# Optimization experiments

Measured on AMD Instinct MI355X. Metric: run time of the kernel, lower is better.

Reference implementation:

```python
import jax, jax.numpy as jnp
import numpy as np

N_QUBITS = 8

def _ry(theta):
    # PennyLane RY = exp(-i theta Y/2) = [[c,-s],[s,c]]
    c = jnp.cos(theta / 2).astype(jnp.complex64)
    s = jnp.sin(theta / 2).astype(jnp.complex64)
    return jnp.stack([jnp.stack([c, -s], -1), jnp.stack([s, c], -1)], -2)

def _rz(theta):
    # PennyLane RZ = diag(e^{-i theta/2}, e^{i theta/2})
    ph = jnp.exp(-0.5j * theta.astype(jnp.complex64))
    z = jnp.zeros_like(ph)
    return jnp.stack([jnp.stack([ph, z], -1), jnp.stack([z, jnp.conj(ph)], -1)], -2)

def _apply_1q(state, U, wire):
    # state: (B, 2,...,2); U: (2,2) or (B,2,2)
    state = jnp.moveaxis(state, wire + 1, -1)
    if U.ndim == 3:
        state = jnp.einsum('bij,b...j->b...i', U, state)
    else:
        state = jnp.einsum('ij,b...j->b...i', U, state)
    return jnp.moveaxis(state, -1, wire + 1)

def _apply_cnot(state, c, t):
    state = jnp.moveaxis(state, (c + 1, t + 1), (-2, -1))
    state = jnp.concatenate([state[..., 0:1, :], state[..., 1:2, ::-1]], axis=-2)
    return jnp.moveaxis(state, (-2, -1), (c + 1, t + 1))

def _circuit(angles, qw):
    # angles: (B, 2*n_qubits), qw: (3, n_qubits, 3)
    B = angles.shape[0]
    state = jnp.zeros((B,) + (2,) * N_QUBITS, jnp.complex64)
    state = state.at[(slice(None),) + (0,) * N_QUBITS].set(1.0)
    for i in range(N_QUBITS):
        state = _apply_1q(state, _ry(angles[:, i]), i)
        state = _apply_1q(state, _rz(angles[:, i + N_QUBITS]), i)
    for layer in range(3):
        for i in range(N_QUBITS):
            phi, theta, omega = qw[layer, i]
            U = _rz(omega) @ _ry(theta) @ _rz(phi)  # Rot(phi,theta,omega)
            state = _apply_1q(state, U, i)
        for i in range(N_QUBITS - 1):
            state = _apply_cnot(state, i, i + 1)
        state = _apply_cnot(state, N_QUBITS - 1, 0)
    probs = jnp.abs(state) ** 2  # (B, 2,...,2) real
    expz = []
    for i in range(N_QUBITS):
        p = probs.sum(axis=tuple(a for a in range(1, N_QUBITS + 1) if a != i + 1))
        expz.append(p[:, 0] - p[:, 1])  # <Z_i> = p(0) - p(1)
    return jnp.stack(expz, -1)


def setup_inputs() -> dict:
    key = jax.random.key(0)
    ks = jax.random.split(key, 10)
    B = 16384
    return {
        'x': jax.random.normal(ks[0], (B, 80), jnp.float32),
        'W1': jax.random.normal(ks[1], (64, 80), jnp.float32) * 0.1,
        'b1': jax.random.normal(ks[2], (64,), jnp.float32) * 0.1,
        'W2': jax.random.normal(ks[3], (32, 64), jnp.float32) * 0.1,
        'b2': jax.random.normal(ks[4], (32,), jnp.float32) * 0.1,
        'W3': jax.random.normal(ks[5], (16, 32), jnp.float32) * 0.1,
        'b3': jax.random.normal(ks[6], (16,), jnp.float32) * 0.1,
        'qw': jax.random.normal(ks[7], (3, 8, 3), jnp.float32),
        'Wp': jax.random.normal(ks[8], (128, 8), jnp.float32) * 0.1,
        'bp': jax.random.normal(ks[9], (128,), jnp.float32) * 0.1,
    }


def reference(x, W1, b1, W2, b2, W3, b3, qw, Wp, bp):
    h = jnp.tanh(x @ W1.T + b1)
    h = jnp.tanh(h @ W2.T + b2)
    angles = h @ W3.T + b3          # (B, 16)
    z = _circuit(angles, qw)        # (B, 8) PauliZ expectations
    return z @ Wp.T + bp            # (B, 128)
```

## Files before the change

### kernel.cpp

```cpp
#include <hip/hip_runtime.h>

typedef float v2f __attribute__((ext_vector_type(2)));

#define WPB 4

__device__ __forceinline__ float xorf(float v, int sb) {
  return __int_as_float(__float_as_int(v) ^ sb);
}

__device__ __forceinline__ void pkfma_ip(v2f a, v2f b, v2f& acc) {
  asm("v_pk_fma_f32 %0, %1, %2, %0" : "+v"(acc) : "v"(a), "v"(b));
}
__device__ __forceinline__ v2f pkmul_bl(v2f c, v2f v) {
  v2f r; asm("v_pk_mul_f32 %0, %1, %2 op_sel:[0,0] op_sel_hi:[0,1]"
             : "=v"(r) : "v"(c), "v"(v)); return r;
}
__device__ __forceinline__ void pkfma_bl(v2f c, v2f v, v2f& acc) {
  asm("v_pk_fma_f32 %0, %1, %2, %0 op_sel:[0,0,0] op_sel_hi:[0,1,1]"
      : "+v"(acc) : "v"(c), "v"(v));
}
__device__ __forceinline__ void pkfma_bl_n(v2f c, v2f v, v2f& acc) {
  asm("v_pk_fma_f32 %0, %1, %2, %0 op_sel:[0,0,0] op_sel_hi:[0,1,1] neg_lo:[1,0,0] neg_hi:[1,0,0]"
      : "+v"(acc) : "v"(c), "v"(v));
}
__device__ __forceinline__ void pkfma_bh_i(v2f c, v2f v, v2f& acc) {
  asm("v_pk_fma_f32 %0, %1, %2, %0 op_sel:[1,1,0] op_sel_hi:[1,0,1] neg_lo:[1,0,0]"
      : "+v"(acc) : "v"(c), "v"(v));
}
__device__ __forceinline__ void pkfma_bh_mi(v2f c, v2f v, v2f& acc) {
  asm("v_pk_fma_f32 %0, %1, %2, %0 op_sel:[1,1,0] op_sel_hi:[1,0,1] neg_hi:[1,0,0]"
      : "+v"(acc) : "v"(c), "v"(v));
}
__device__ __forceinline__ v2f cmul(v2f a, v2f b) {
  v2f r = pkmul_bl(a, b);
  pkfma_bh_i(a, b, r);
  return r;
}

template<int M>
__device__ __forceinline__ float xch(float v, int a32) {
  if constexpr (M == 32)
    return __int_as_float(__builtin_amdgcn_ds_bpermute(a32, __float_as_int(v)));
  else if constexpr (M == 16 || M == 4)
    return __int_as_float(__builtin_amdgcn_ds_swizzle(__float_as_int(v), (M << 10) | 0x1f));
  else if constexpr (M == 8) {
    int i = __float_as_int(v);
    return __int_as_float(__builtin_amdgcn_update_dpp(i, i, 0x128, 0xF, 0xF, false));
  } else if constexpr (M == 2) {
    int i = __float_as_int(v);
    return __int_as_float(__builtin_amdgcn_update_dpp(i, i, 0x4E, 0xF, 0xF, false));
  } else {
    int i = __float_as_int(v);
    return __int_as_float(__builtin_amdgcn_update_dpp(i, i, 0xB1, 0xF, 0xF, false));
  }
}
template<int M>
__device__ __forceinline__ v2f xch2(v2f v, int a32) {
  v2f r; r.x = xch<M>(v.x, a32); r.y = xch<M>(v.y, a32); return r;
}
__device__ __forceinline__ v2f bperm2(int addr, v2f v) {
  v2f r;
  r.x = __int_as_float(__builtin_amdgcn_ds_bpermute(addr, __float_as_int(v.x)));
  r.y = __int_as_float(__builtin_amdgcn_ds_bpermute(addr, __float_as_int(v.y)));
  return r;
}

__device__ __forceinline__ void gpair(v2f& a, v2f& b, v2f P1, v2f P2) {
  v2f na = pkmul_bl(P1, a);
  pkfma_bh_i(P1, a, na);
  pkfma_bl(P2, b, na);
  pkfma_bh_i(P2, b, na);
  v2f nb = pkmul_bl(P1, b);
  pkfma_bh_mi(P1, b, nb);
  pkfma_bl_n(P2, a, nb);
  pkfma_bh_i(P2, a, nb);
  a = na; b = nb;
}
__device__ __forceinline__ v2f glane(v2f a, v2f p, v2f P1, v2f P2) {
  v2f t = pkmul_bl(P1, a);
  pkfma_bh_i(P1, a, t);
  pkfma_bl(P2, p, t);
  pkfma_bh_i(P2, p, t);
  return t;
}

template<int W>
__device__ __forceinline__ void gate_both(v2f* SA, v2f* SB, v2f P1, v2f P2,
                                          const int* sb, int a32) {
  if constexpr (W == 0) {
    gpair(SA[0], SA[2], P1, P2); gpair(SA[1], SA[3], P1, P2);
    gpair(SB[0], SB[2], P1, P2); gpair(SB[1], SB[3], P1, P2);
  } else if constexpr (W == 1) {
    gpair(SA[0], SA[1], P1, P2); gpair(SA[2], SA[3], P1, P2);
    gpair(SB[0], SB[1], P1, P2); gpair(SB[2], SB[3], P1, P2);
  } else {
    constexpr int M = 1 << (7 - W);
    const int s = sb[W - 2];
    v2f P1s = P1; P1s.y = xorf(P1.y, s);
    v2f P2s = P2; P2s.x = xorf(P2.x, s);
    v2f pa0 = xch2<M>(SA[0], a32), pa1 = xch2<M>(SA[1], a32),
        pa2 = xch2<M>(SA[2], a32), pa3 = xch2<M>(SA[3], a32);
    v2f pb0 = xch2<M>(SB[0], a32), pb1 = xch2<M>(SB[1], a32),
        pb2 = xch2<M>(SB[2], a32), pb3 = xch2<M>(SB[3], a32);
    SA[0] = glane(SA[0], pa0, P1s, P2s); SA[1] = glane(SA[1], pa1, P1s, P2s);
    SA[2] = glane(SA[2], pa2, P1s, P2s); SA[3] = glane(SA[3], pa3, P1s, P2s);
    SB[0] = glane(SB[0], pb0, P1s, P2s); SB[1] = glane(SB[1], pb1, P1s, P2s);
    SB[2] = glane(SB[2], pb2, P1s, P2s); SB[3] = glane(SB[3], pb3, P1s, P2s);
  }
}

__device__ __forceinline__ void build_state(v2f* S, const float4* csW, int lane) {
  v2f g[6];
  #pragma unroll
  for (int w = 2; w < 8; ++w) {
    float4 c = csW[w];
    v2f P1 = (v2f){c.x, c.y};
    v2f nc2 = (v2f){-c.z, c.w};
    bool shi = ((lane >> (7 - w)) & 1) != 0;
    g[w - 2] = shi ? nc2 : P1;
  }
  v2f c23 = cmul(g[0], g[1]);
  v2f c45 = cmul(g[2], g[3]);
  v2f c67 = cmul(g[4], g[5]);
  v2f common = cmul(c23, cmul(c45, c67));
  float4 c0 = csW[0], c1 = csW[1];
  v2f P10 = (v2f){c0.x, c0.y}, m0 = (v2f){-c0.z, c0.w};
  v2f P11 = (v2f){c1.x, c1.y}, m1 = (v2f){-c1.z, c1.w};
  S[0] = cmul(cmul(P10, P11), common);
  S[1] = cmul(cmul(P10, m1 ), common);
  S[2] = cmul(cmul(m0 , P11), common);
  S[3] = cmul(cmul(m0 , m1 ), common);
}

__device__ __forceinline__ void cnot_ring(v2f* S, int addrA, int addrB, int lane) {
  { v2f t = S[2]; S[2] = S[3]; S[3] = t; }
  S[0] = bperm2(addrA, S[0]); S[2] = bperm2(addrA, S[2]);
  S[1] = bperm2(addrB, S[1]); S[3] = bperm2(addrB, S[3]);
  bool c0 = (lane & 1) != 0;
  v2f t0 = S[0], t1 = S[1];
  S[0] = c0 ? S[2] : S[0]; S[2] = c0 ? t0 : S[2];
  S[1] = c0 ? S[3] : S[1]; S[3] = c0 ? t1 : S[3];
}

__device__ __forceinline__ void readout(const v2f* S, int lane, const int* sb,
                                        int a32, float* z) {
  float p0 = S[0].x*S[0].x + S[0].y*S[0].y;
  float p1 = S[1].x*S[1].x + S[1].y*S[1].y;
  float p2 = S[2].x*S[2].x + S[2].y*S[2].y;
  float p3 = S[3].x*S[3].x + S[3].y*S[3].y;
  float E = (p0 + p3) - (p1 + p2);
  float F = (p0 + p2) - (p1 + p3);
  float Fv = xorf(F, (__popc(lane) & 1) << 31);
  float Sm = E, d1, d2, d3, d4, d5, d6;
  { float p = xch<32>(Sm, a32); d1 = xorf(Sm - p, sb[0]); Sm += p; }
  { float p = xch<16>(Sm, a32); Sm += p;
    float q = xch<16>(d1, a32); d2 = xorf(d1 - q, sb[1]); d1 += q; }
  { float p = xch<8>(Sm, a32); Sm += p;
    float q = xch<8>(d1, a32); d1 += q;
    float r = xch<8>(d2, a32); d3 = xorf(d2 - r, sb[2]); d2 += r; }
  { float p = xch<4>(Sm, a32); Sm += p;
    float q = xch<4>(d1, a32); d1 += q;
    float r = xch<4>(d2, a32); d2 += r;
    float t = xch<4>(d3, a32); d4 = xorf(d3 - t, sb[3]); d3 += t; }
  { float p = xch<2>(Sm, a32); Sm += p;
    float q = xch<2>(d1, a32); d1 += q;
    float r = xch<2>(d2, a32); d2 += r;
    float t = xch<2>(d3, a32); d3 += t;
    float w = xch<2>(d4, a32); d5 = xorf(d4 - w, sb[4]); d4 += w; }
  { float p = xch<1>(Sm, a32); Sm += p;
    float q = xch<1>(d1, a32); d1 += q;
    float r = xch<1>(d2, a32); d2 += r;
    float t = xch<1>(d3, a32); d3 += t;
    float w = xch<1>(d4, a32); d4 += w;
    float v = xch<1>(d5, a32); d6 = xorf(d5 - v, sb[5]); d5 += v; }
  Fv += xch<32>(Fv, a32); Fv += xch<16>(Fv, a32); Fv += xch<8>(Fv, a32);
  Fv += xch<4>(Fv, a32);  Fv += xch<2>(Fv, a32);  Fv += xch<1>(Fv, a32);
  z[0] = Fv; z[1] = Sm; z[2] = d1; z[3] = d2;
  z[4] = d3; z[5] = d4; z[6] = d5; z[7] = d6;
}

__device__ __forceinline__ float fast_tanh(float x) {
  float e = __expf(2.f * x);
  return 1.f - 2.f * __builtin_amdgcn_rcpf(e + 1.f);
}
__device__ __forceinline__ v2f vlo(float4 v) { return (v2f){v.x, v.y}; }
__device__ __forceinline__ v2f vhi(float4 v) { return (v2f){v.z, v.w}; }

__global__ void prep_rot_kernel(const float* __restrict__ qw, float* __restrict__ U) {
  int t = threadIdx.x;
  if (t < 24) {
    float phi = qw[t*3+0], theta = qw[t*3+1], omega = qw[t*3+2];
    float st, ct; sincosf(0.5f*theta, &st, &ct);
    float sa, ca; sincosf(0.5f*(phi+omega), &sa, &ca);
    float sd, cd; sincosf(0.5f*(phi-omega), &sd, &cd);
    float4 o; o.x = ct*ca; o.y = -ct*sa; o.z = -st*cd; o.w = -st*sd;
    ((float4*)U)[t] = o;
  }
}

__global__ __launch_bounds__(64*WPB) void qblock_kernel(
    const float* __restrict__ x,  const float* __restrict__ W1, const float* __restrict__ b1,
    const float* __restrict__ W2, const float* __restrict__ b2,
    const float* __restrict__ W3, const float* __restrict__ b3,
    const float* __restrict__ Urot, const float* __restrict__ Wp, const float* __restrict__ bp,
    float* __restrict__ out, int B2)
{
  __shared__ float  h1s[WPB][2][64];
  __shared__ float  h2s[WPB][2][32];
  __shared__ v2f    cs [WPB][2][16];
  __shared__ float4 csW[WPB][2][8];

  const int lane = threadIdx.x & 63;
  const int wv   = threadIdx.x >> 6;
  int bw = blockIdx.x * WPB + wv;
  if (bw >= B2) bw = B2 - 1;
  bw = __builtin_amdgcn_readfirstlane(bw);
  const int e0 = 2 * bw, e1 = e0 + 1;
  const v2f* Ug2 = (const v2f*)Urot;

  {
    const float4* xv0 = (const float4*)(x + (size_t)e0 * 80);
    const float4* xv1 = (const float4*)(x + (size_t)e1 * 80);
    const float4* wr  = (const float4*)(W1 + lane * 80);
    float bv = b1[lane];
    v2f a00 = (v2f){bv, 0.f}, a01 = (v2f){0.f, 0.f};
    v2f a10 = (v2f){bv, 0.f}, a11 = (v2f){0.f, 0.f};
    #pragma unroll
    for (int k = 0; k < 20; ++k) {
      float4 wk = wr[k], x0 = xv0[k], x1 = xv1[k];
      pkfma_ip(vlo(x0), vlo(wk), a00); pkfma_ip(vhi(x0), vhi(wk), a01);
      pkfma_ip(vlo(x1), vlo(wk), a10); pkfma_ip(vhi(x1), vhi(wk), a11);
    }
    h1s[wv][0][lane] = fast_tanh((a00.x + a00.y) + (a01.x + a01.y));
    h1s[wv][1][lane] = fast_tanh((a10.x + a10.y) + (a11.x + a11.y));
  }
  __threadfence_block();

  {
    const int e = lane >> 5, row = lane & 31;
    const float4* hv = (const float4*)(&h1s[wv][e][0]);
    const float4* wr = (const float4*)(W2 + row * 64);
    v2f ac0 = (v2f){b2[row], 0.f}, ac1 = (v2f){0.f, 0.f};
    #pragma unroll
    for (int k = 0; k < 16; ++k) {
      float4 hk = hv[k], wk = wr[k];
      pkfma_ip(vlo(hk), vlo(wk), ac0);
      pkfma_ip(vhi(hk), vhi(wk), ac1);
    }
    h2s[wv][e][row] = fast_tanh((ac0.x + ac0.y) + (ac1.x + ac1.y));
  }
  __threadfence_block();

  if (lane < 32) {
    const int e = lane >> 4, row = lane & 15;
    const float4* hv = (const float4*)(&h2s[wv][e][0]);
    const float4* wr = (const float4*)(W3 + row * 32);
    v2f ac0 = (v2f){b3[row], 0.f}, ac1 = (v2f){0.f, 0.f};
    #pragma unroll
    for (int k = 0; k < 8; ++k) {
      float4 hk = hv[k], wk = wr[k];
      pkfma_ip(vlo(hk), vlo(wk), ac0);
      pkfma_ip(vhi(hk), vhi(wk), ac1);
    }
    float sh, ch; __sincosf(0.5f * ((ac0.x + ac0.y) + (ac1.x + ac1.y)), &sh, &ch);
    cs[wv][e][row] = (v2f){ch, sh};
  }
  __threadfence_block();

  if (lane < 32) {
    const int e = lane >> 4, k = lane & 15;
    if (k < 8) {
      v2f yy = cs[wv][e][k], zz = cs[wv][e][k + 8];
      v2f u1 = (v2f){  yy.x * zz.x, -yy.x * zz.y };
      v2f u2 = (v2f){ -yy.y * zz.x,  yy.y * zz.y };
      v2f cu1 = (v2f){ u1.x, -u1.y };
      v2f cu2 = (v2f){ u2.x, -u2.y };
      v2f r1 = Ug2[2 * k], r2 = Ug2[2 * k + 1];
      v2f P1c = cmul(r1, u1);
      pkfma_bl_n(r2, cu2, P1c);
      pkfma_bh_mi(r2, cu2, P1c);
      v2f P2c = cmul(r1, u2);
      pkfma_bl(r2, cu1, P2c);
      pkfma_bh_i(r2, cu1, P2c);
      csW[wv][e][k] = make_float4(P1c.x, P1c.y, P2c.x, P2c.y);
    }
  }
  __threadfence_block();

  const int a32 = (lane ^ 32) << 2;
  const int sb[6] = { (lane&32)<<26, (lane&16)<<27, (lane&8)<<28,
                      (lane&4)<<29, (lane&2)<<30, (lane&1)<<31 };
  const int addrA = ((lane ^ (lane >> 1)) & 63) << 2;
  const int addrB = addrA ^ 128;

  v2f SA[4], SB[4];
  build_state(SA, &csW[wv][0][0], lane);
  build_state(SB, &csW[wv][1][0], lane);
  cnot_ring(SA, addrA, addrB, lane); cnot_ring(SB, addrA, addrB, lane);

  #define LGB(l, i) { v2f P1 = Ug2[((l)*8+(i))*2], P2 = Ug2[((l)*8+(i))*2+1]; \
    gate_both<i>(SA, SB, P1, P2, sb, a32); }
  LGB(1,0) LGB(1,1) LGB(1,2) LGB(1,3) LGB(1,4) LGB(1,5) LGB(1,6) LGB(1,7)
  cnot_ring(SA, addrA, addrB, lane); cnot_ring(SB, addrA, addrB, lane);
  LGB(2,0) LGB(2,1) LGB(2,2) LGB(2,3) LGB(2,4) LGB(2,5) LGB(2,6) LGB(2,7)
  #undef LGB

  float zA[8], zB[8];
  readout(SA, lane, sb, a32, zA);
  readout(SB, lane, sb, a32, zB);

  const int r0 = 2 * lane;
  const float4* wp = (const float4*)(Wp + r0 * 8);
  float4 w0v = wp[0], w1v = wp[1], w2v = wp[2], w3v = wp[3];
  float2 bpv = ((const float2*)bp)[lane];
  {
    float o0 = bpv.x + zA[0]*w0v.x + zA[1]*w0v.y + zA[2]*w0v.z + zA[3]*w0v.w
                     + zA[4]*w1v.x + zA[5]*w1v.y + zA[6]*w1v.z + zA[7]*w1v.w;
    float o1 = bpv.y + zA[0]*w2v.x + zA[1]*w2v.y + zA[2]*w2v.z + zA[3]*w2v.w
                     + zA[4]*w3v.x + zA[5]*w3v.y + zA[6]*w3v.z + zA[7]*w3v.w;
    ((float2*)(out + (size_t)e0 * 128))[lane] = make_float2(o0, o1);
  }
  {
    float o0 = bpv.x + zB[0]*w0v.x + zB[1]*w0v.y + zB[2]*w0v.z + zB[3]*w0v.w
                     + zB[4]*w1v.x + zB[5]*w1v.y + zB[6]*w1v.z + zB[7]*w1v.w;
    float o1 = bpv.y + zB[0]*w2v.x + zB[1]*w2v.y + zB[2]*w2v.z + zB[3]*w2v.w
                     + zB[4]*w3v.x + zB[5]*w3v.y + zB[6]*w3v.z + zB[7]*w3v.w;
    ((float2*)(out + (size_t)e1 * 128))[lane] = make_float2(o0, o1);
  }
}

extern "C" void kernel_launch(void* const* d_in, const int* in_sizes, int n_in,
                              void* d_out, int out_size, void* d_ws, size_t ws_size,
                              hipStream_t stream) {
  const float* x  = (const float*)d_in[0];
  const float* W1 = (const float*)d_in[1];
  const float* b1 = (const float*)d_in[2];
  const float* W2 = (const float*)d_in[3];
  const float* b2 = (const float*)d_in[4];
  const float* W3 = (const float*)d_in[5];
  const float* b3 = (const float*)d_in[6];
  const float* qw = (const float*)d_in[7];
  const float* Wp = (const float*)d_in[8];
  const float* bp = (const float*)d_in[9];
  float* out = (float*)d_out;
  float* Urot = (float*)d_ws;

  const int B = in_sizes[0] / 80;
  const int B2 = B / 2;
  prep_rot_kernel<<<1, 64, 0, stream>>>(qw, Urot);
  const int grid = (B2 + WPB - 1) / WPB;
  qblock_kernel<<<grid, 64 * WPB, 0, stream>>>(x, W1, b1, W2, b2, W3, b3,
                                               Urot, Wp, bp, out, B2);
}
```

Baseline: 47.88 us.

## Process four batch elements per wavefront instead of two

Each wavefront now simulates four circuits at once, widening per-lane state to 16 complex pairs. The first MLP layer reuses each W1 row load across four samples, and later stages use all lanes instead of half. This is meant to amortize weight loads and gate-parameter broadcasts and to add independent work for latency hiding. It raises register pressure, may reduce occupancy, and halves the grid size.

```diff
diff --git a/kernel.cpp b/kernel.cpp
--- a/kernel.cpp
+++ b/kernel.cpp
@@ -3,6 +3,7 @@
 typedef float v2f __attribute__((ext_vector_type(2)));
 
 #define WPB 4
+#define NE  4
 
 __device__ __forceinline__ float xorf(float v, int sb) {
   return __int_as_float(__float_as_int(v) ^ sb);
@@ -85,27 +86,32 @@
 }
 
 template<int W>
-__device__ __forceinline__ void gate_both(v2f* SA, v2f* SB, v2f P1, v2f P2,
-                                          const int* sb, int a32) {
+__device__ __forceinline__ void gate_all(v2f* S, v2f P1, v2f P2,
+                                         const int* sb, int a32) {
   if constexpr (W == 0) {
-    gpair(SA[0], SA[2], P1, P2); gpair(SA[1], SA[3], P1, P2);
-    gpair(SB[0], SB[2], P1, P2); gpair(SB[1], SB[3], P1, P2);
+    #pragma unroll
+    for (int e = 0; e < NE; ++e) {
+      gpair(S[4*e+0], S[4*e+2], P1, P2); gpair(S[4*e+1], S[4*e+3], P1, P2);
+    }
   } else if constexpr (W == 1) {
-    gpair(SA[0], SA[1], P1, P2); gpair(SA[2], SA[3], P1, P2);
-    gpair(SB[0], SB[1], P1, P2); gpair(SB[2], SB[3], P1, P2);
+    #pragma unroll
+    for (int e = 0; e < NE; ++e) {
+      gpair(S[4*e+0], S[4*e+1], P1, P2); gpair(S[4*e+2], S[4*e+3], P1, P2);
+    }
   } else {
     constexpr int M = 1 << (7 - W);
     const int s = sb[W - 2];
     v2f P1s = P1; P1s.y = xorf(P1.y, s);
     v2f P2s = P2; P2s.x = xorf(P2.x, s);
-    v2f pa0 = xch2<M>(SA[0], a32), pa1 = xch2<M>(SA[1], a32),
-        pa2 = xch2<M>(SA[2], a32), pa3 = xch2<M>(SA[3], a32);
-    v2f pb0 = xch2<M>(SB[0], a32), pb1 = xch2<M>(SB[1], a32),
-        pb2 = xch2<M>(SB[2], a32), pb3 = xch2<M>(SB[3], a32);
-    SA[0] = glane(SA[0], pa0, P1s, P2s); SA[1] = glane(SA[1], pa1, P1s, P2s);
-    SA[2] = glane(SA[2], pa2, P1s, P2s); SA[3] = glane(SA[3], pa3, P1s, P2s);
-    SB[0] = glane(SB[0], pb0, P1s, P2s); SB[1] = glane(SB[1], pb1, P1s, P2s);
-    SB[2] = glane(SB[2], pb2, P1s, P2s); SB[3] = glane(SB[3], pb3, P1s, P2s);
+    #pragma unroll
+    for (int e = 0; e < NE; ++e) {
+      v2f p0 = xch2<M>(S[4*e+0], a32), p1 = xch2<M>(S[4*e+1], a32),
+          p2 = xch2<M>(S[4*e+2], a32), p3 = xch2<M>(S[4*e+3], a32);
+      S[4*e+0] = glane(S[4*e+0], p0, P1s, P2s);
+      S[4*e+1] = glane(S[4*e+1], p1, P1s, P2s);
+      S[4*e+2] = glane(S[4*e+2], p2, P1s, P2s);
+      S[4*e+3] = glane(S[4*e+3], p3, P1s, P2s);
+    }
   }
 }
 
@@ -203,55 +209,62 @@
     const float* __restrict__ W2, const float* __restrict__ b2,
     const float* __restrict__ W3, const float* __restrict__ b3,
     const float* __restrict__ Urot, const float* __restrict__ Wp, const float* __restrict__ bp,
-    float* __restrict__ out, int B2)
+    float* __restrict__ out, int B4)
 {
-  __shared__ float  h1s[WPB][2][64];
-  __shared__ float  h2s[WPB][2][32];
-  __shared__ v2f    cs [WPB][2][16];
-  __shared__ float4 csW[WPB][2][8];
+  __shared__ float  h1s[WPB][NE][64];
+  __shared__ float  h2s[WPB][NE][32];
+  __shared__ v2f    cs [WPB][NE][16];
+  __shared__ float4 csW[WPB][NE][8];
 
   const int lane = threadIdx.x & 63;
   const int wv   = threadIdx.x >> 6;
   int bw = blockIdx.x * WPB + wv;
-  if (bw >= B2) bw = B2 - 1;
+  if (bw >= B4) bw = B4 - 1;
   bw = __builtin_amdgcn_readfirstlane(bw);
-  const int e0 = 2 * bw, e1 = e0 + 1;
+  const int e0 = NE * bw;
   const v2f* Ug2 = (const v2f*)Urot;
 
   {
-    const float4* xv0 = (const float4*)(x + (size_t)e0 * 80);
-    const float4* xv1 = (const float4*)(x + (size_t)e1 * 80);
-    const float4* wr  = (const float4*)(W1 + lane * 80);
+    const float4* wr = (const float4*)(W1 + lane * 80);
     float bv = b1[lane];
-    v2f a00 = (v2f){bv, 0.f}, a01 = (v2f){0.f, 0.f};
-    v2f a10 = (v2f){bv, 0.f}, a11 = (v2f){0.f, 0.f};
+    v2f a0[NE], a1[NE];
+    #pragma unroll
+    for (int e = 0; e < NE; ++e) { a0[e] = (v2f){bv, 0.f}; a1[e] = (v2f){0.f, 0.f}; }
     #pragma unroll
     for (int k = 0; k < 20; ++k) {
-      float4 wk = wr[k], x0 = xv0[k], x1 = xv1[k];
-      pkfma_ip(vlo(x0), vlo(wk), a00); pkfma_ip(vhi(x0), vhi(wk), a01);
-      pkfma_ip(vlo(x1), vlo(wk), a10); pkfma_ip(vhi(x1), vhi(wk), a11);
-    }
-    h1s[wv][0][lane] = fast_tanh((a00.x + a00.y) + (a01.x + a01.y));
-    h1s[wv][1][lane] = fast_tanh((a10.x + a10.y) + (a11.x + a11.y));
+      float4 wk = wr[k];
+      #pragma unroll
+      for (int e = 0; e < NE; ++e) {
+        float4 xk = ((const float4*)(x + (size_t)(e0 + e) * 80))[k];
+        pkfma_ip(vlo(xk), vlo(wk), a0[e]);
+        pkfma_ip(vhi(xk), vhi(wk), a1[e]);
+      }
+    }
+    #pragma unroll
+    for (int e = 0; e < NE; ++e)
+      h1s[wv][e][lane] = fast_tanh((a0[e].x + a0[e].y) + (a1[e].x + a1[e].y));
   }
   __threadfence_block();
 
   {
-    const int e = lane >> 5, row = lane & 31;
-    const float4* hv = (const float4*)(&h1s[wv][e][0]);
+    const int ep = lane >> 5, row = lane & 31;
     const float4* wr = (const float4*)(W2 + row * 64);
-    v2f ac0 = (v2f){b2[row], 0.f}, ac1 = (v2f){0.f, 0.f};
+    const float4* hvA = (const float4*)(&h1s[wv][2*ep+0][0]);
+    const float4* hvB = (const float4*)(&h1s[wv][2*ep+1][0]);
+    v2f aA0 = (v2f){b2[row], 0.f}, aA1 = (v2f){0.f, 0.f};
+    v2f aB0 = aA0, aB1 = aA1;
     #pragma unroll
     for (int k = 0; k < 16; ++k) {
-      float4 hk = hv[k], wk = wr[k];
-      pkfma_ip(vlo(hk), vlo(wk), ac0);
-      pkfma_ip(vhi(hk), vhi(wk), ac1);
-    }
-    h2s[wv][e][row] = fast_tanh((ac0.x + ac0.y) + (ac1.x + ac1.y));
+      float4 wk = wr[k], hA = hvA[k], hB = hvB[k];
+      pkfma_ip(vlo(hA), vlo(wk), aA0); pkfma_ip(vhi(hA), vhi(wk), aA1);
+      pkfma_ip(vlo(hB), vlo(wk), aB0); pkfma_ip(vhi(hB), vhi(wk), aB1);
+    }
+    h2s[wv][2*ep+0][row] = fast_tanh((aA0.x + aA0.y) + (aA1.x + aA1.y));
+    h2s[wv][2*ep+1][row] = fast_tanh((aB0.x + aB0.y) + (aB1.x + aB1.y));
   }
   __threadfence_block();
 
-  if (lane < 32) {
+  {
     const int e = lane >> 4, row = lane & 15;
     const float4* hv = (const float4*)(&h2s[wv][e][0]);
     const float4* wr = (const float4*)(W3 + row * 32);
@@ -268,22 +281,20 @@
   __threadfence_block();
 
   if (lane < 32) {
-    const int e = lane >> 4, k = lane & 15;
-    if (k < 8) {
-      v2f yy = cs[wv][e][k], zz = cs[wv][e][k + 8];
-      v2f u1 = (v2f){  yy.x * zz.x, -yy.x * zz.y };
-      v2f u2 = (v2f){ -yy.y * zz.x,  yy.y * zz.y };
-      v2f cu1 = (v2f){ u1.x, -u1.y };
-      v2f cu2 = (v2f){ u2.x, -u2.y };
-      v2f r1 = Ug2[2 * k], r2 = Ug2[2 * k + 1];
-      v2f P1c = cmul(r1, u1);
-      pkfma_bl_n(r2, cu2, P1c);
-      pkfma_bh_mi(r2, cu2, P1c);
-      v2f P2c = cmul(r1, u2);
-      pkfma_bl(r2, cu1, P2c);
-      pkfma_bh_i(r2, cu1, P2c);
-      csW[wv][e][k] = make_float4(P1c.x, P1c.y, P2c.x, P2c.y);
-    }
+    const int e = lane >> 3, k = lane & 7;
+    v2f yy = cs[wv][e][k], zz = cs[wv][e][k + 8];
+    v2f u1 = (v2f){  yy.x * zz.x, -yy.x * zz.y };
+    v2f u2 = (v2f){ -yy.y * zz.x,  yy.y * zz.y };
+    v2f cu1 = (v2f){ u1.x, -u1.y };
+    v2f cu2 = (v2f){ u2.x, -u2.y };
+    v2f r1 = Ug2[2 * k], r2 = Ug2[2 * k + 1];
+    v2f P1c = cmul(r1, u1);
+    pkfma_bl_n(r2, cu2, P1c);
+    pkfma_bh_mi(r2, cu2, P1c);
+    v2f P2c = cmul(r1, u2);
+    pkfma_bl(r2, cu1, P2c);
+    pkfma_bh_i(r2, cu1, P2c);
+    csW[wv][e][k] = make_float4(P1c.x, P1c.y, P2c.x, P2c.y);
   }
   __threadfence_block();
 
@@ -293,39 +304,33 @@
   const int addrA = ((lane ^ (lane >> 1)) & 63) << 2;
   const int addrB = addrA ^ 128;
 
-  v2f SA[4], SB[4];
-  build_state(SA, &csW[wv][0][0], lane);
-  build_state(SB, &csW[wv][1][0], lane);
-  cnot_ring(SA, addrA, addrB, lane); cnot_ring(SB, addrA, addrB, lane);
+  v2f S[4 * NE];
+  #pragma unroll
+  for (int e = 0; e < NE; ++e) build_state(&S[4*e], &csW[wv][e][0], lane);
+  #pragma unroll
+  for (int e = 0; e < NE; ++e) cnot_ring(&S[4*e], addrA, addrB, lane);
 
   #define LGB(l, i) { v2f P1 = Ug2[((l)*8+(i))*2], P2 = Ug2[((l)*8+(i))*2+1]; \
-    gate_both<i>(SA, SB, P1, P2, sb, a32); }
+    gate_all<i>(S, P1, P2, sb, a32); }
   LGB(1,0) LGB(1,1) LGB(1,2) LGB(1,3) LGB(1,4) LGB(1,5) LGB(1,6) LGB(1,7)
-  cnot_ring(SA, addrA, addrB, lane); cnot_ring(SB, addrA, addrB, lane);
+  #pragma unroll
+  for (int e = 0; e < NE; ++e) cnot_ring(&S[4*e], addrA, addrB, lane);
   LGB(2,0) LGB(2,1) LGB(2,2) LGB(2,3) LGB(2,4) LGB(2,5) LGB(2,6) LGB(2,7)
   #undef LGB
-
-  float zA[8], zB[8];
-  readout(SA, lane, sb, a32, zA);
-  readout(SB, lane, sb, a32, zB);
 
   const int r0 = 2 * lane;
   const float4* wp = (const float4*)(Wp + r0 * 8);
   float4 w0v = wp[0], w1v = wp[1], w2v = wp[2], w3v = wp[3];
   float2 bpv = ((const float2*)bp)[lane];
-  {
-    float o0 = bpv.x + zA[0]*w0v.x + zA[1]*w0v.y + zA[2]*w0v.z + zA[3]*w0v.w
-                     + zA[4]*w1v.x + zA[5]*w1v.y + zA[6]*w1v.z + zA[7]*w1v.w;
-    float o1 = bpv.y + zA[0]*w2v.x + zA[1]*w2v.y + zA[2]*w2v.z + zA[3]*w2v.w
-                     + zA[4]*w3v.x + zA[5]*w3v.y + zA[6]*w3v.z + zA[7]*w3v.w;
-    ((float2*)(out + (size_t)e0 * 128))[lane] = make_float2(o0, o1);
-  }
-  {
-    float o0 = bpv.x + zB[0]*w0v.x + zB[1]*w0v.y + zB[2]*w0v.z + zB[3]*w0v.w
-                     + zB[4]*w1v.x + zB[5]*w1v.y + zB[6]*w1v.z + zB[7]*w1v.w;
-    float o1 = bpv.y + zB[0]*w2v.x + zB[1]*w2v.y + zB[2]*w2v.z + zB[3]*w2v.w
-                     + zB[4]*w3v.x + zB[5]*w3v.y + zB[6]*w3v.z + zB[7]*w3v.w;
-    ((float2*)(out + (size_t)e1 * 128))[lane] = make_float2(o0, o1);
+  #pragma unroll
+  for (int e = 0; e < NE; ++e) {
+    float z[8];
+    readout(&S[4*e], lane, sb, a32, z);
+    float o0 = bpv.x + z[0]*w0v.x + z[1]*w0v.y + z[2]*w0v.z + z[3]*w0v.w
+                     + z[4]*w1v.x + z[5]*w1v.y + z[6]*w1v.z + z[7]*w1v.w;
+    float o1 = bpv.y + z[0]*w2v.x + z[1]*w2v.y + z[2]*w2v.z + z[3]*w2v.w
+                     + z[4]*w3v.x + z[5]*w3v.y + z[6]*w3v.z + z[7]*w3v.w;
+    ((float2*)(out + (size_t)(e0 + e) * 128))[lane] = make_float2(o0, o1);
   }
 }
 
@@ -346,9 +351,9 @@
   float* Urot = (float*)d_ws;
 
   const int B = in_sizes[0] / 80;
-  const int B2 = B / 2;
+  const int B4 = B / NE;
   prep_rot_kernel<<<1, 64, 0, stream>>>(qw, Urot);
-  const int grid = (B2 + WPB - 1) / WPB;
+  const int grid = (B4 + WPB - 1) / WPB;
   qblock_kernel<<<grid, 64 * WPB, 0, stream>>>(x, W1, b1, W2, b2, W3, b3,
-                                               Urot, Wp, bp, out, B2);
-}
+                                               Urot, Wp, bp, out, B4);
+}
```

New measurement: 42.20 us. 11.9% less time.
